# Performance work log

Hardware: AMD Instinct MI355X
Metric: run time of the kernel (lower is better)

## Reference

```python
import jax, jax.numpy as jnp
import numpy as np

N_NODES = 40960
N_EDGES = 655360
IN_DIM = 128
HID = 128
HEADS = 4
CH = HID // HEADS  # per-head channels = 32
N_GRAPHS = 16
NEG_SLOPE = 0.2


def setup_inputs() -> dict:
    key = jax.random.key(0)
    ks = jax.random.split(key, 32)
    inp = {
        "x": jax.random.normal(ks[0], (N_NODES, IN_DIM), dtype=jnp.float32),
        "edge_index": jax.random.randint(ks[1], (2, N_EDGES), 0, N_NODES, dtype=jnp.int64),
        "batch_vec": jnp.sort(jax.random.randint(ks[2], (N_NODES,), 0, N_GRAPHS, dtype=jnp.int64)),
    }
    dims = [(IN_DIM, HID), (HID, HID), (HID, HID)]
    ki = 3
    for l, (din, dout) in enumerate(dims):
        s = 1.0 / np.sqrt(din)
        inp[f"Wl{l}"] = jax.random.normal(ks[ki + 0], (din, dout), dtype=jnp.float32) * s
        inp[f"bl{l}"] = jnp.zeros((dout,), dtype=jnp.float32)
        inp[f"Wr{l}"] = jax.random.normal(ks[ki + 1], (din, dout), dtype=jnp.float32) * s
        inp[f"br{l}"] = jnp.zeros((dout,), dtype=jnp.float32)
        inp[f"att{l}"] = jax.random.normal(ks[ki + 2], (HEADS, CH), dtype=jnp.float32) * (1.0 / np.sqrt(CH))
        inp[f"b{l}"] = jnp.zeros((dout,), dtype=jnp.float32)
        ki += 3
    return inp


def _gatv2_layer(x, src, dst, Wl, bl, Wr, br, att, bias):
    # GATv2Conv (PyG semantics, add_self_loops=True handled by caller's src/dst)
    n = x.shape[0]
    xl = (x @ Wl + bl).reshape(n, HEADS, CH)  # source transform
    xr = (x @ Wr + br).reshape(n, HEADS, CH)  # destination transform
    m = xl[src] + xr[dst]                      # [E, H, C]
    e = jnp.einsum("ehc,hc->eh", jax.nn.leaky_relu(m, NEG_SLOPE), att)  # [E, H]
    emax = jax.ops.segment_max(e, dst, num_segments=n)
    ex = jnp.exp(e - emax[dst])
    denom = jax.ops.segment_sum(ex, dst, num_segments=n)
    alpha = ex / denom[dst]                    # segment softmax over in-edges
    out = jax.ops.segment_sum(alpha[:, :, None] * xl[src], dst, num_segments=n)
    return out.reshape(n, HEADS * CH) + bias


def reference(x, edge_index, batch_vec,
              Wl0, bl0, Wr0, br0, att0, b0,
              Wl1, bl1, Wr1, br1, att1, b1,
              Wl2, bl2, Wr2, br2, att2, b2):
    n = x.shape[0]
    loops = jnp.arange(n, dtype=edge_index.dtype)
    src = jnp.concatenate([edge_index[0], loops])  # PyG default add_self_loops=True
    dst = jnp.concatenate([edge_index[1], loops])

    h = _gatv2_layer(x, src, dst, Wl0, bl0, Wr0, br0, att0, b0)
    h = jax.nn.relu(h)
    h = _gatv2_layer(h, src, dst, Wl1, bl1, Wr1, br1, att1, b1)
    h = jax.nn.relu(h)
    h = _gatv2_layer(h, src, dst, Wl2, bl2, Wr2, br2, att2, b2)

    # global_mean_pool over batch assignment
    sums = jax.ops.segment_sum(h, batch_vec, num_segments=N_GRAPHS)
    cnt = jax.ops.segment_sum(jnp.ones((n,), dtype=h.dtype), batch_vec, num_segments=N_GRAPHS)
    pooled = sums / jnp.maximum(cnt, 1.0)[:, None]
    return pooled, h
```

## Files before the change

### kernel.cpp

```cpp
#include <hip/hip_runtime.h>

#define NN 40960
#define NE 655360
#define ET (NE + NN)
#define D 128
#define NG 16
#define PL 16896
#define NREP 8

typedef unsigned int u32;
typedef unsigned short u16;
typedef long long i64;
typedef __attribute__((ext_vector_type(8))) short bf8v;
typedef __attribute__((ext_vector_type(4))) float f4v;

struct P18 { const void* p[18]; };

__device__ __forceinline__ float bf2f(u16 v){ return __uint_as_float(((u32)v)<<16); }
__device__ __forceinline__ u16 f2bf(float f){
  u32 u = __float_as_uint(f);
  return (u16)((u + 0x7FFFu + ((u>>16)&1u)) >> 16);
}
__device__ __forceinline__ int geti(const void* p, long long i, int f64, int bound){
  long long v = f64 ? ((const i64*)p)[i] : (long long)((const int*)p)[i];
  int x = (int)v;
  return (x < 0) ? 0 : ((x >= bound) ? bound-1 : x);
}
__device__ __forceinline__ void stf(void* p, long long i, float v, int isbf){
  if (isbf) ((u16*)p)[i] = f2bf(v); else ((float*)p)[i] = v;
}
__device__ __forceinline__ float rdf(const void* p, long long i, int isbf){
  return isbf ? bf2f(((const u16*)p)[i]) : ((const float*)p)[i];
}
__device__ __forceinline__ float4 ldb4(const u16* p){
  ushort4 u = *(const ushort4*)p;
  return make_float4(bf2f(u.x), bf2f(u.y), bf2f(u.z), bf2f(u.w));
}

__global__ void k_setup(const void* __restrict__ ei, const void* __restrict__ x,
                        int* __restrict__ flags, u32* __restrict__ cursor, float* __restrict__ pool,
                        u16* __restrict__ csr){
  int b = blockIdx.x;
  if (b == 0){
    __shared__ int nz, cnt;
    if (threadIdx.x == 0){ nz = 0; cnt = 0; }
    __syncthreads();
    if (((const int*)ei)[2*threadIdx.x + 1] != 0) atomicAdd(&nz, 1);
    if (threadIdx.x < 128){
      u16 v = ((const u16*)x)[2*threadIdx.x];
      int ex = (v >> 7) & 0xFF;
      if (ex >= 100 && ex <= 140) atomicAdd(&cnt, 1);
    }
    __syncthreads();
    if (threadIdx.x == 0){
      flags[0] = (nz == 0) ? 1 : 0;
      flags[1] = (cnt >= 64) ? 1 : 0;
    }
  } else if (b <= 1280){
    cursor[(b-1)*256 + threadIdx.x] = 0u;
  } else if (b <= 1288){
    int i = (b-1281)*256 + threadIdx.x;
    if (i < NG*D) pool[i] = 0.f;
  } else {
    if (threadIdx.x < 16) csr[ET + threadIdx.x] = 0;
  }
}

__global__ void k_prep(P18 ps, const void* __restrict__ x, u16* __restrict__ xb,
                       float* __restrict__ prm, const int* __restrict__ flags){
  int b = blockIdx.x;
  int isbf = flags[1];
  if (b >= 390){
    long long i = (long long)(b - 390)*256 + threadIdx.x;
    xb[i] = f2bf(rdf(x, i, isbf));
    return;
  }
  int l = b / 130;
  int i = (b % 130)*256 + threadIdx.x;
  const void* Wl  = ps.p[6*l+0];
  const void* bl  = ps.p[6*l+1];
  const void* Wr  = ps.p[6*l+2];
  const void* br  = ps.p[6*l+3];
  const void* att = ps.p[6*l+4];
  const void* bb  = ps.p[6*l+5];
  float* p = prm + (size_t)l*PL;
  if (i < 32768){
    int n = i >> 7, k = i & 127;
    float v = (n < 128) ? rdf(Wl, k*128 + n, isbf) : rdf(Wr, k*128 + (n - 128), isbf);
    ((u16*)p)[i] = f2bf(v);
    return;
  }
  float* fb = p + 16384;
  if (i < 33024){ int gc = i - 32768; fb[gc] = (gc < 128) ? rdf(bl, gc, isbf) : rdf(br, gc - 128, isbf); }
  else if (i < 33152) fb[256 + (i - 33024)] = rdf(att, i - 33024, isbf);
  else                fb[384 + (i - 33152)] = rdf(bb, i - 33152, isbf);
}

__global__ void k_hist(const void* __restrict__ ei, u32* __restrict__ cursor, const int* __restrict__ flags){
  int e = blockIdx.x*256 + threadIdx.x;
  if (e >= ET) return;
  int dd = (e < NE) ? geti(ei, (long long)NE + e, flags[0], NN) : e - NE;
  atomicAdd(&cursor[(e & (NREP-1))*NN + dd], 1u);
}

__global__ __launch_bounds__(256) void k_scanA(u32* __restrict__ cursor, u32* __restrict__ tot,
                                               u32* __restrict__ psum){
  __shared__ u32 red[256];
  int t = threadIdx.x;
  int dd = blockIdx.x*256 + t;
  u32 run = 0;
  #pragma unroll
  for (int r = 0; r < NREP; ++r){
    u32 v = cursor[r*NN + dd];
    cursor[r*NN + dd] = run;
    run += v;
  }
  tot[dd] = run;
  red[t] = run;
  __syncthreads();
  #pragma unroll
  for (int off = 128; off > 0; off >>= 1){
    if (t < off) red[t] += red[t + off];
    __syncthreads();
  }
  if (t == 0) psum[blockIdx.x] = red[0];
}

__global__ __launch_bounds__(256) void k_scanB(u32* __restrict__ psum, u32* __restrict__ offs,
                                               const void* __restrict__ batch, u32* __restrict__ bnd,
                                               const int* __restrict__ flags){
  __shared__ u32 sh[256];
  int t = threadIdx.x;
  sh[t] = (t < 160) ? psum[t] : 0u;
  __syncthreads();
  #pragma unroll
  for (int off = 1; off < 256; off <<= 1){
    u32 add = (t >= off) ? sh[t - off] : 0u;
    __syncthreads();
    sh[t] += add;
    __syncthreads();
  }
  if (t < 160) psum[t] = (t == 0) ? 0u : sh[t - 1];
  if (t == 160) offs[NN] = sh[159];
  if (t >= 192 && t <= 192 + NG){
    int g = t - 192;
    if (g == NG){ bnd[NG] = NN; }
    else {
      int f = flags[0];
      int lo = 0, hi = NN;
      while (lo < hi){
        int mid = (lo + hi) >> 1;
        if (geti(batch, mid, f, NG) < g) lo = mid + 1; else hi = mid;
      }
      bnd[g] = (u32)lo;
    }
  }
}

__global__ __launch_bounds__(256) void k_scanC(u32* __restrict__ cursor, u32* __restrict__ offs,
                                               const u32* __restrict__ tot, const u32* __restrict__ psum){
  __shared__ u32 sh[256];
  int t = threadIdx.x;
  int dd = blockIdx.x*256 + t;
  u32 v = tot[dd];
  sh[t] = v;
  __syncthreads();
  #pragma unroll
  for (int off = 1; off < 256; off <<= 1){
    u32 add = (t >= off) ? sh[t - off] : 0u;
    __syncthreads();
    sh[t] += add;
    __syncthreads();
  }
  u32 excl = ((t > 0) ? sh[t - 1] : 0u) + psum[blockIdx.x];
  offs[dd] = excl;
  #pragma unroll
  for (int r = 0; r < NREP; ++r)
    cursor[r*NN + dd] += excl;
}

__global__ void k_scatter(const void* __restrict__ ei, u32* __restrict__ cursor,
                          u16* __restrict__ csr, const int* __restrict__ flags){
  int e = blockIdx.x*256 + threadIdx.x;
  if (e >= ET) return;
  int f = flags[0];
  int s, dd;
  if (e < NE){ s = geti(ei, e, f, NN); dd = geti(ei, (long long)NE + e, f, NN); }
  else { s = dd = e - NE; }
  u32 pos = atomicAdd(&cursor[(e & (NREP-1))*NN + dd], 1u);
  csr[pos] = (u16)s;
}

__global__ __launch_bounds__(256) void k_gemm(const u16* __restrict__ Xb, const float* __restrict__ pr,
                                              u16* __restrict__ xl, u16* __restrict__ xr)
{
  int wv = threadIdx.x >> 6, lane = threadIdx.x & 63;
  int row0 = blockIdx.x*64 + wv*16;
  int rA = lane & 15, ks = lane >> 4;
  const u16* wt     = (const u16*)pr;
  const float* bias = pr + 16384;

  const u16* xp = Xb + (size_t)(row0 + rA)*D + ks*8;
  bf8v a0 = *(const bf8v*)(xp);
  bf8v a1 = *(const bf8v*)(xp + 32);
  bf8v a2 = *(const bf8v*)(xp + 64);
  bf8v a3 = *(const bf8v*)(xp + 96);

  int n0 = blockIdx.y*4;
  #pragma unroll
  for (int t = 0; t < 4; ++t, ++n0){
    int gc = n0*16 + rA;
    const u16* wp = wt + (size_t)gc*D + ks*8;
    bf8v b0 = *(const bf8v*)(wp);
    bf8v b1 = *(const bf8v*)(wp + 32);
    bf8v b2 = *(const bf8v*)(wp + 64);
    bf8v b3 = *(const bf8v*)(wp + 96);
    float bv = bias[gc];
    f4v acc = {bv, bv, bv, bv};
    acc = __builtin_amdgcn_mfma_f32_16x16x32_bf16(a0, b0, acc, 0, 0, 0);
    acc = __builtin_amdgcn_mfma_f32_16x16x32_bf16(a1, b1, acc, 0, 0, 0);
    acc = __builtin_amdgcn_mfma_f32_16x16x32_bf16(a2, b2, acc, 0, 0, 0);
    acc = __builtin_amdgcn_mfma_f32_16x16x32_bf16(a3, b3, acc, 0, 0, 0);
    u16* dst = (gc < 128) ? xl : xr;
    int cc = (gc < 128) ? gc : gc - 128;
    #pragma unroll
    for (int r = 0; r < 4; ++r)
      dst[(size_t)(row0 + ks*4 + r)*D + cc] = f2bf(acc[r]);
  }
}

__global__ __launch_bounds__(256) void k_node(const u16* __restrict__ xl, const u16* __restrict__ xr,
    const u32* __restrict__ offs, const u16* __restrict__ csr, const float* __restrict__ pr,
    u16* __restrict__ hb, float* __restrict__ hf, void* __restrict__ out,
    const int* __restrict__ flags, int last)
{
  int node = blockIdx.x*4 + (threadIdx.x >> 6);
  int lane = threadIdx.x & 63;
  int half = lane >> 5;
  int c = (lane & 31) * 4;
  const u16* xlc = xl + c;
  float4 xrv  = ldb4(xr + (size_t)node*D + c);
  float4 attv = *(const float4*)(pr + 16640 + c);
  u32 j0 = offs[node], j1 = offs[node + 1];

  float mx = -1e30f, ssum = 0.f;
  float4 acc = make_float4(0.f, 0.f, 0.f, 0.f);

  u32 j = j0 + half;
  u32 o0 = ((u32)csr[j]) << 7, o1 = ((u32)csr[j+2]) << 7;
  float4 g0 = ldb4(xlc + o0);
  float4 g1 = ldb4(xlc + o1);
  u32 o2 = ((u32)csr[j+4]) << 7, o3 = ((u32)csr[j+6]) << 7;

  for (; j < j1; j += 4){
    float4 n0 = ldb4(xlc + o2);
    float4 n1 = ldb4(xlc + o3);
    u32 t0 = ((u32)csr[j+8]) << 7, t1 = ((u32)csr[j+10]) << 7;

    {
      float m, p;
      m = g0.x + xrv.x; p = fmaxf(m, 0.2f*m) * attv.x;
      m = g0.y + xrv.y; p = fmaf(fmaxf(m, 0.2f*m), attv.y, p);
      m = g0.z + xrv.z; p = fmaf(fmaxf(m, 0.2f*m), attv.z, p);
      m = g0.w + xrv.w; p = fmaf(fmaxf(m, 0.2f*m), attv.w, p);
      p += __shfl_xor(p, 1, 64);
      p += __shfl_xor(p, 2, 64);
      p += __shfl_xor(p, 4, 64);
      if (p > mx + 8.f){
        float eo = __expf(mx - p);
        ssum  *= eo;
        acc.x *= eo; acc.y *= eo; acc.z *= eo; acc.w *= eo;
        mx = p;
      }
      float en = __expf(p - mx);
      ssum += en;
      acc.x = fmaf(en, g0.x, acc.x);
      acc.y = fmaf(en, g0.y, acc.y);
      acc.z = fmaf(en, g0.z, acc.z);
      acc.w = fmaf(en, g0.w, acc.w);
    }
    if (j + 2 < j1){
      float m, p;
      m = g1.x + xrv.x; p = fmaxf(m, 0.2f*m) * attv.x;
      m = g1.y + xrv.y; p = fmaf(fmaxf(m, 0.2f*m), attv.y, p);
      m = g1.z + xrv.z; p = fmaf(fmaxf(m, 0.2f*m), attv.z, p);
      m = g1.w + xrv.w; p = fmaf(fmaxf(m, 0.2f*m), attv.w, p);
      p += __shfl_xor(p, 1, 64);
      p += __shfl_xor(p, 2, 64);
      p += __shfl_xor(p, 4, 64);
      if (p > mx + 8.f){
        float eo = __expf(mx - p);
        ssum  *= eo;
        acc.x *= eo; acc.y *= eo; acc.z *= eo; acc.w *= eo;
        mx = p;
      }
      float en = __expf(p - mx);
      ssum += en;
      acc.x = fmaf(en, g1.x, acc.x);
      acc.y = fmaf(en, g1.y, acc.y);
      acc.z = fmaf(en, g1.z, acc.z);
      acc.w = fmaf(en, g1.w, acc.w);
    }
    g0 = n0; g1 = n1; o2 = t0; o3 = t1;
  }

  float mo = __shfl_xor(mx, 32, 64);
  float so = __shfl_xor(ssum, 32, 64);
  float ax = __shfl_xor(acc.x, 32, 64);
  float ay = __shfl_xor(acc.y, 32, 64);
  float az = __shfl_xor(acc.z, 32, 64);
  float aw = __shfl_xor(acc.w, 32, 64);
  float n  = fmaxf(mx, mo);
  float e0 = __expf(mx - n), e1 = __expf(mo - n);
  ssum  = ssum*e0 + so*e1;
  acc.x = acc.x*e0 + ax*e1;
  acc.y = acc.y*e0 + ay*e1;
  acc.z = acc.z*e0 + az*e1;
  acc.w = acc.w*e0 + aw*e1;

  if (half == 0){
    float inv = 1.0f / fmaxf(ssum, 1e-30f);
    float4 bv = *(const float4*)(pr + 16768 + c);
    float4 v = make_float4(acc.x*inv + bv.x, acc.y*inv + bv.y,
                           acc.z*inv + bv.z, acc.w*inv + bv.w);
    if (!last){
      v.x = fmaxf(v.x, 0.f); v.y = fmaxf(v.y, 0.f);
      v.z = fmaxf(v.z, 0.f); v.w = fmaxf(v.w, 0.f);
      ushort4 o = make_ushort4(f2bf(v.x), f2bf(v.y), f2bf(v.z), f2bf(v.w));
      *(ushort4*)(hb + (size_t)node*D + c) = o;
    } else {
      *(float4*)(hf + (size_t)node*D + c) = v;
      int isbf = flags[1];
      long long o = (long long)NG*D + (long long)node*D + c;
      stf(out, o+0, v.x, isbf); stf(out, o+1, v.y, isbf);
      stf(out, o+2, v.z, isbf); stf(out, o+3, v.w, isbf);
    }
  }
}

__global__ __launch_bounds__(256) void k_pool1(const float* __restrict__ h, const u32* __restrict__ bnd,
                                               float* __restrict__ pool){
  __shared__ float red[256];
  int g = blockIdx.x >> 4, sl = blockIdx.x & 15;
  int ch = threadIdx.x & 127, ro = threadIdx.x >> 7;
  u32 b0 = bnd[g], b1 = bnd[g + 1];
  float acc = 0.f;
  for (u32 r = b0 + sl*2 + ro; r < b1; r += 32) acc += h[(size_t)r*D + ch];
  red[threadIdx.x] = acc;
  __syncthreads();
  if (threadIdx.x < 128)
    unsafeAtomicAdd(&pool[g*D + ch], red[threadIdx.x] + red[threadIdx.x + 128]);
}

__global__ void k_pool2(const float* __restrict__ pool, const u32* __restrict__ bnd,
                        void* __restrict__ out, const int* __restrict__ flags){
  int i = blockIdx.x*256 + threadIdx.x;
  if (i >= NG*D) return;
  int g = i >> 7;
  float c = (float)(bnd[g + 1] - bnd[g]);
  stf(out, i, pool[i] / fmaxf(c, 1.f), flags[1]);
}

extern "C" void kernel_launch(void* const* d_in, const int* in_sizes, int n_in,
                              void* d_out, int out_size, void* d_ws, size_t ws_size,
                              hipStream_t stream) {
  const void* x     = d_in[0];
  const void* ei    = d_in[1];
  const void* batch = d_in[2];

  const long long nf = (long long)NN*D + 3*PL + NG*D;
  const long long nh = (long long)NN*D*3;
  const long long nu = (NN + 1) + (long long)NREP*NN + NN + (NG + 1) + 160 + 2;
  const long long nc = ET + 16;
  if (ws_size < (size_t)nf*4 + (size_t)nh*2 + (size_t)nu*4 + (size_t)nc*2 + 256) return;

  float* ws    = (float*)d_ws;
  float* xf    = ws;
  u16*  xb    = (u16*)(xf + (size_t)NN*D);
  u16*  xl    = xb + (size_t)NN*D;
  u16*  xr    = xl + (size_t)NN*D;
  float* prm   = (float*)(xr + (size_t)NN*D);
  float* pool  = prm + 3*PL;
  u32*  offs   = (u32*)(pool + NG*D);
  u32*  cursor = offs + (NN + 1);
  u32*  tot    = cursor + (size_t)NREP*NN;
  u32*  bnd    = tot + NN;
  u32*  psum   = bnd + (NG + 1);
  int*  flags  = (int*)(psum + 160);
  u16*  csr    = (u16*)(flags + 2);

  k_setup<<<1290, 256, 0, stream>>>(ei, x, flags, cursor, pool, csr);
  P18 ps;
  for (int i = 0; i < 18; ++i) ps.p[i] = d_in[3 + i];
  k_prep<<<390 + (NN*D)/256, 256, 0, stream>>>(ps, x, xb, prm, flags);

  k_hist<<<ET/256, 256, 0, stream>>>(ei, cursor, flags);
  k_scanA<<<160, 256, 0, stream>>>(cursor, tot, psum);
  k_scanB<<<1, 256, 0, stream>>>(psum, offs, batch, bnd, flags);
  k_scanC<<<160, 256, 0, stream>>>(cursor, offs, tot, psum);
  k_scatter<<<ET/256, 256, 0, stream>>>(ei, cursor, csr, flags);

  for (int l = 0; l < 3; ++l){
    const float* p = prm + (size_t)l*PL;
    k_gemm<<<dim3(NN/64, 4), 256, 0, stream>>>(xb, p, xl, xr);
    k_node<<<NN/4, 256, 0, stream>>>(xl, xr, offs, csr, p, xb, xf, d_out, flags, l == 2);
  }
  k_pool1<<<NG*16, 256, 0, stream>>>(xf, bnd, pool);
  k_pool2<<<8, 256, 0, stream>>>(pool, bnd, d_out, flags);
}
```

Baseline: 313.8 us.

## Fuse histogram into prep, scatter with first GEMM; widen node lanes to 8 channels

The edge-degree histogram now runs as extra blocks of the prep kernel, and the CSR scatter shares a launch with the layer-0 projection GEMM. This removes two kernel launches and lets the independent work overlap. The node aggregation kernel now gives each lane 8 channels and runs 4 edge groups per wavefront instead of 2, with a two-step shuffle merge at the end. That roughly halves the shuffles per edge and issues wider gathers, at the cost of more registers and a longer final reduction.

After: 303.4 us. 3.3% less time.

```diff
diff --git a/kernel.cpp b/kernel.cpp
--- a/kernel.cpp
+++ b/kernel.cpp
@@ -7,6 +7,7 @@
 #define NG 16
 #define PL 16896
 #define NREP 8
+#define SCB 2720
 
 typedef unsigned int u32;
 typedef unsigned short u16;
@@ -67,9 +68,18 @@
 }
 
 __global__ void k_prep(P18 ps, const void* __restrict__ x, u16* __restrict__ xb,
-                       float* __restrict__ prm, const int* __restrict__ flags){
+                       float* __restrict__ prm, const void* __restrict__ ei,
+                       u32* __restrict__ cursor, const int* __restrict__ flags){
   int b = blockIdx.x;
   int isbf = flags[1];
+  if (b >= 20870){
+    int e = (b - 20870)*256 + threadIdx.x;
+    if (e < ET){
+      int dd = (e < NE) ? geti(ei, (long long)NE + e, flags[0], NN) : e - NE;
+      atomicAdd(&cursor[(e & (NREP-1))*NN + dd], 1u);
+    }
+    return;
+  }
   if (b >= 390){
     long long i = (long long)(b - 390)*256 + threadIdx.x;
     xb[i] = f2bf(rdf(x, i, isbf));
@@ -96,13 +106,6 @@
   else                fb[384 + (i - 33152)] = rdf(bb, i - 33152, isbf);
 }
 
-__global__ void k_hist(const void* __restrict__ ei, u32* __restrict__ cursor, const int* __restrict__ flags){
-  int e = blockIdx.x*256 + threadIdx.x;
-  if (e >= ET) return;
-  int dd = (e < NE) ? geti(ei, (long long)NE + e, flags[0], NN) : e - NE;
-  atomicAdd(&cursor[(e & (NREP-1))*NN + dd], 1u);
-}
-
 __global__ __launch_bounds__(256) void k_scanA(u32* __restrict__ cursor, u32* __restrict__ tot,
                                                u32* __restrict__ psum){
   __shared__ u32 red[256];
@@ -179,23 +182,12 @@
     cursor[r*NN + dd] += excl;
 }
 
-__global__ void k_scatter(const void* __restrict__ ei, u32* __restrict__ cursor,
-                          u16* __restrict__ csr, const int* __restrict__ flags){
-  int e = blockIdx.x*256 + threadIdx.x;
-  if (e >= ET) return;
-  int f = flags[0];
-  int s, dd;
-  if (e < NE){ s = geti(ei, e, f, NN); dd = geti(ei, (long long)NE + e, f, NN); }
-  else { s = dd = e - NE; }
-  u32 pos = atomicAdd(&cursor[(e & (NREP-1))*NN + dd], 1u);
-  csr[pos] = (u16)s;
-}
-
-__global__ __launch_bounds__(256) void k_gemm(const u16* __restrict__ Xb, const float* __restrict__ pr,
-                                              u16* __restrict__ xl, u16* __restrict__ xr)
+__device__ __forceinline__ void gemm_body(int bx, int by, int tid,
+    const u16* __restrict__ Xb, const float* __restrict__ pr,
+    u16* __restrict__ xl, u16* __restrict__ xr)
 {
-  int wv = threadIdx.x >> 6, lane = threadIdx.x & 63;
-  int row0 = blockIdx.x*64 + wv*16;
+  int wv = tid >> 6, lane = tid & 63;
+  int row0 = bx*64 + wv*16;
   int rA = lane & 15, ks = lane >> 4;
   const u16* wt     = (const u16*)pr;
   const float* bias = pr + 16384;
@@ -206,7 +198,7 @@
   bf8v a2 = *(const bf8v*)(xp + 64);
   bf8v a3 = *(const bf8v*)(xp + 96);
 
-  int n0 = blockIdx.y*4;
+  int n0 = by*4;
   #pragma unroll
   for (int t = 0; t < 4; ++t, ++n0){
     int gc = n0*16 + rA;
@@ -229,6 +221,32 @@
   }
 }
 
+__global__ __launch_bounds__(256) void k_gemm(const u16* __restrict__ Xb, const float* __restrict__ pr,
+                                              u16* __restrict__ xl, u16* __restrict__ xr){
+  gemm_body(blockIdx.x, blockIdx.y, threadIdx.x, Xb, pr, xl, xr);
+}
+
+__global__ __launch_bounds__(256) void k_scatgemm(const void* __restrict__ ei, u32* __restrict__ cursor,
+    u16* __restrict__ csr, const int* __restrict__ flags,
+    const u16* __restrict__ Xb, const float* __restrict__ pr,
+    u16* __restrict__ xl, u16* __restrict__ xr)
+{
+  int b = blockIdx.x;
+  if (b < SCB){
+    int e = b*256 + threadIdx.x;
+    if (e >= ET) return;
+    int f = flags[0];
+    int s, dd;
+    if (e < NE){ s = geti(ei, e, f, NN); dd = geti(ei, (long long)NE + e, f, NN); }
+    else { s = dd = e - NE; }
+    u32 pos = atomicAdd(&cursor[(e & (NREP-1))*NN + dd], 1u);
+    csr[pos] = (u16)s;
+    return;
+  }
+  int g = b - SCB;
+  gemm_body(g % 640, g / 640, threadIdx.x, Xb, pr, xl, xr);
+}
+
 __global__ __launch_bounds__(256) void k_node(const u16* __restrict__ xl, const u16* __restrict__ xr,
     const u32* __restrict__ offs, const u16* __restrict__ csr, const float* __restrict__ pr,
     u16* __restrict__ hb, float* __restrict__ hf, void* __restrict__ out,
@@ -236,104 +254,98 @@
 {
   int node = blockIdx.x*4 + (threadIdx.x >> 6);
   int lane = threadIdx.x & 63;
-  int half = lane >> 5;
-  int c = (lane & 31) * 4;
+  int g2 = lane >> 4;
+  int c = (lane & 15) * 8;
   const u16* xlc = xl + c;
-  float4 xrv  = ldb4(xr + (size_t)node*D + c);
-  float4 attv = *(const float4*)(pr + 16640 + c);
+  const u16* xrp = xr + (size_t)node*D + c;
+  float4 xr0 = ldb4(xrp), xr1 = ldb4(xrp + 4);
+  float4 at0 = *(const float4*)(pr + 16640 + c);
+  float4 at1 = *(const float4*)(pr + 16640 + c + 4);
   u32 j0 = offs[node], j1 = offs[node + 1];
 
   float mx = -1e30f, ssum = 0.f;
-  float4 acc = make_float4(0.f, 0.f, 0.f, 0.f);
-
-  u32 j = j0 + half;
-  u32 o0 = ((u32)csr[j]) << 7, o1 = ((u32)csr[j+2]) << 7;
-  float4 g0 = ldb4(xlc + o0);
-  float4 g1 = ldb4(xlc + o1);
-  u32 o2 = ((u32)csr[j+4]) << 7, o3 = ((u32)csr[j+6]) << 7;
+  float4 ac0 = make_float4(0.f,0.f,0.f,0.f), ac1 = make_float4(0.f,0.f,0.f,0.f);
+
+  u32 j = j0 + g2;
+  u32 oc = ((u32)csr[j]) << 7;
+  float4 g0 = ldb4(xlc + oc), g1 = ldb4(xlc + oc + 4);
+  u32 on = ((u32)csr[j + 4]) << 7;
 
   for (; j < j1; j += 4){
-    float4 n0 = ldb4(xlc + o2);
-    float4 n1 = ldb4(xlc + o3);
-    u32 t0 = ((u32)csr[j+8]) << 7, t1 = ((u32)csr[j+10]) << 7;
-
-    {
-      float m, p;
-      m = g0.x + xrv.x; p = fmaxf(m, 0.2f*m) * attv.x;
-      m = g0.y + xrv.y; p = fmaf(fmaxf(m, 0.2f*m), attv.y, p);
-      m = g0.z + xrv.z; p = fmaf(fmaxf(m, 0.2f*m), attv.z, p);
-      m = g0.w + xrv.w; p = fmaf(fmaxf(m, 0.2f*m), attv.w, p);
-      p += __shfl_xor(p, 1, 64);
-      p += __shfl_xor(p, 2, 64);
-      p += __shfl_xor(p, 4, 64);
-      if (p > mx + 8.f){
-        float eo = __expf(mx - p);
-        ssum  *= eo;
-        acc.x *= eo; acc.y *= eo; acc.z *= eo; acc.w *= eo;
-        mx = p;
-      }
-      float en = __expf(p - mx);
-      ssum += en;
-      acc.x = fmaf(en, g0.x, acc.x);
-      acc.y = fmaf(en, g0.y, acc.y);
-      acc.z = fmaf(en, g0.z, acc.z);
-      acc.w = fmaf(en, g0.w, acc.w);
-    }
-    if (j + 2 < j1){
-      float m, p;
-      m = g1.x + xrv.x; p = fmaxf(m, 0.2f*m) * attv.x;
-      m = g1.y + xrv.y; p = fmaf(fmaxf(m, 0.2f*m), attv.y, p);
-      m = g1.z + xrv.z; p = fmaf(fmaxf(m, 0.2f*m), attv.z, p);
-      m = g1.w + xrv.w; p = fmaf(fmaxf(m, 0.2f*m), attv.w, p);
-      p += __shfl_xor(p, 1, 64);
-      p += __shfl_xor(p, 2, 64);
-      p += __shfl_xor(p, 4, 64);
-      if (p > mx + 8.f){
-        float eo = __expf(mx - p);
-        ssum  *= eo;
-        acc.x *= eo; acc.y *= eo; acc.z *= eo; acc.w *= eo;
-        mx = p;
-      }
-      float en = __expf(p - mx);
-      ssum += en;
-      acc.x = fmaf(en, g1.x, acc.x);
-      acc.y = fmaf(en, g1.y, acc.y);
-      acc.z = fmaf(en, g1.z, acc.z);
-      acc.w = fmaf(en, g1.w, acc.w);
-    }
-    g0 = n0; g1 = n1; o2 = t0; o3 = t1;
-  }
-
-  float mo = __shfl_xor(mx, 32, 64);
-  float so = __shfl_xor(ssum, 32, 64);
-  float ax = __shfl_xor(acc.x, 32, 64);
-  float ay = __shfl_xor(acc.y, 32, 64);
-  float az = __shfl_xor(acc.z, 32, 64);
-  float aw = __shfl_xor(acc.w, 32, 64);
-  float n  = fmaxf(mx, mo);
-  float e0 = __expf(mx - n), e1 = __expf(mo - n);
-  ssum  = ssum*e0 + so*e1;
-  acc.x = acc.x*e0 + ax*e1;
-  acc.y = acc.y*e0 + ay*e1;
-  acc.z = acc.z*e0 + az*e1;
-  acc.w = acc.w*e0 + aw*e1;
-
-  if (half == 0){
+    float4 n0 = ldb4(xlc + on), n1 = ldb4(xlc + on + 4);
+    u32 o2 = ((u32)csr[j + 8]) << 7;
+
+    float m, p;
+    m = g0.x + xr0.x; p = fmaxf(m, 0.2f*m) * at0.x;
+    m = g0.y + xr0.y; p = fmaf(fmaxf(m, 0.2f*m), at0.y, p);
+    m = g0.z + xr0.z; p = fmaf(fmaxf(m, 0.2f*m), at0.z, p);
+    m = g0.w + xr0.w; p = fmaf(fmaxf(m, 0.2f*m), at0.w, p);
+    m = g1.x + xr1.x; p = fmaf(fmaxf(m, 0.2f*m), at1.x, p);
+    m = g1.y + xr1.y; p = fmaf(fmaxf(m, 0.2f*m), at1.y, p);
+    m = g1.z + xr1.z; p = fmaf(fmaxf(m, 0.2f*m), at1.z, p);
+    m = g1.w + xr1.w; p = fmaf(fmaxf(m, 0.2f*m), at1.w, p);
+    p += __shfl_xor(p, 1, 64);
+    p += __shfl_xor(p, 2, 64);
+    if (p > mx + 8.f){
+      float eo = __expf(mx - p);
+      ssum *= eo;
+      ac0.x *= eo; ac0.y *= eo; ac0.z *= eo; ac0.w *= eo;
+      ac1.x *= eo; ac1.y *= eo; ac1.z *= eo; ac1.w *= eo;
+      mx = p;
+    }
+    float en = __expf(p - mx);
+    ssum += en;
+    ac0.x = fmaf(en, g0.x, ac0.x); ac0.y = fmaf(en, g0.y, ac0.y);
+    ac0.z = fmaf(en, g0.z, ac0.z); ac0.w = fmaf(en, g0.w, ac0.w);
+    ac1.x = fmaf(en, g1.x, ac1.x); ac1.y = fmaf(en, g1.y, ac1.y);
+    ac1.z = fmaf(en, g1.z, ac1.z); ac1.w = fmaf(en, g1.w, ac1.w);
+    g0 = n0; g1 = n1; on = o2;
+  }
+
+  #pragma unroll
+  for (int off = 16; off < 64; off <<= 1){
+    float mo  = __shfl_xor(mx, off, 64);
+    float so  = __shfl_xor(ssum, off, 64);
+    float b0x = __shfl_xor(ac0.x, off, 64), b0y = __shfl_xor(ac0.y, off, 64);
+    float b0z = __shfl_xor(ac0.z, off, 64), b0w = __shfl_xor(ac0.w, off, 64);
+    float b1x = __shfl_xor(ac1.x, off, 64), b1y = __shfl_xor(ac1.y, off, 64);
+    float b1z = __shfl_xor(ac1.z, off, 64), b1w = __shfl_xor(ac1.w, off, 64);
+    float nm = fmaxf(mx, mo);
+    float e0 = __expf(mx - nm), e1 = __expf(mo - nm);
+    ssum  = ssum*e0 + so*e1;
+    ac0.x = ac0.x*e0 + b0x*e1; ac0.y = ac0.y*e0 + b0y*e1;
+    ac0.z = ac0.z*e0 + b0z*e1; ac0.w = ac0.w*e0 + b0w*e1;
+    ac1.x = ac1.x*e0 + b1x*e1; ac1.y = ac1.y*e0 + b1y*e1;
+    ac1.z = ac1.z*e0 + b1z*e1; ac1.w = ac1.w*e0 + b1w*e1;
+    mx = nm;
+  }
+
+  if (lane < 16){
     float inv = 1.0f / fmaxf(ssum, 1e-30f);
-    float4 bv = *(const float4*)(pr + 16768 + c);
-    float4 v = make_float4(acc.x*inv + bv.x, acc.y*inv + bv.y,
-                           acc.z*inv + bv.z, acc.w*inv + bv.w);
+    float4 bv0 = *(const float4*)(pr + 16768 + c);
+    float4 bv1 = *(const float4*)(pr + 16768 + c + 4);
+    float4 v0 = make_float4(ac0.x*inv + bv0.x, ac0.y*inv + bv0.y,
+                            ac0.z*inv + bv0.z, ac0.w*inv + bv0.w);
+    float4 v1 = make_float4(ac1.x*inv + bv1.x, ac1.y*inv + bv1.y,
+                            ac1.z*inv + bv1.z, ac1.w*inv + bv1.w);
     if (!last){
-      v.x = fmaxf(v.x, 0.f); v.y = fmaxf(v.y, 0.f);
-      v.z = fmaxf(v.z, 0.f); v.w = fmaxf(v.w, 0.f);
-      ushort4 o = make_ushort4(f2bf(v.x), f2bf(v.y), f2bf(v.z), f2bf(v.w));
-      *(ushort4*)(hb + (size_t)node*D + c) = o;
+      v0.x = fmaxf(v0.x, 0.f); v0.y = fmaxf(v0.y, 0.f);
+      v0.z = fmaxf(v0.z, 0.f); v0.w = fmaxf(v0.w, 0.f);
+      v1.x = fmaxf(v1.x, 0.f); v1.y = fmaxf(v1.y, 0.f);
+      v1.z = fmaxf(v1.z, 0.f); v1.w = fmaxf(v1.w, 0.f);
+      u16* hp = hb + (size_t)node*D + c;
+      *(ushort4*)(hp)     = make_ushort4(f2bf(v0.x), f2bf(v0.y), f2bf(v0.z), f2bf(v0.w));
+      *(ushort4*)(hp + 4) = make_ushort4(f2bf(v1.x), f2bf(v1.y), f2bf(v1.z), f2bf(v1.w));
     } else {
-      *(float4*)(hf + (size_t)node*D + c) = v;
+      float* fp = hf + (size_t)node*D + c;
+      *(float4*)(fp)     = v0;
+      *(float4*)(fp + 4) = v1;
       int isbf = flags[1];
       long long o = (long long)NG*D + (long long)node*D + c;
-      stf(out, o+0, v.x, isbf); stf(out, o+1, v.y, isbf);
-      stf(out, o+2, v.z, isbf); stf(out, o+3, v.w, isbf);
+      stf(out, o+0, v0.x, isbf); stf(out, o+1, v0.y, isbf);
+      stf(out, o+2, v0.z, isbf); stf(out, o+3, v0.w, isbf);
+      stf(out, o+4, v1.x, isbf); stf(out, o+5, v1.y, isbf);
+      stf(out, o+6, v1.z, isbf); stf(out, o+7, v1.w, isbf);
     }
   }
 }
@@ -392,18 +404,19 @@
   k_setup<<<1290, 256, 0, stream>>>(ei, x, flags, cursor, pool, csr);
   P18 ps;
   for (int i = 0; i < 18; ++i) ps.p[i] = d_in[3 + i];
-  k_prep<<<390 + (NN*D)/256, 256, 0, stream>>>(ps, x, xb, prm, flags);
-
-  k_hist<<<ET/256, 256, 0, stream>>>(ei, cursor, flags);
+  k_prep<<<390 + (NN*D)/256 + SCB, 256, 0, stream>>>(ps, x, xb, prm, ei, cursor, flags);
+
   k_scanA<<<160, 256, 0, stream>>>(cursor, tot, psum);
   k_scanB<<<1, 256, 0, stream>>>(psum, offs, batch, bnd, flags);
   k_scanC<<<160, 256, 0, stream>>>(cursor, offs, tot, psum);
-  k_scatter<<<ET/256, 256, 0, stream>>>(ei, cursor, csr, flags);
+  k_scatgemm<<<SCB + 2560, 256, 0, stream>>>(ei, cursor, csr, flags,
+                                             xb, prm, xl, xr);
 
   for (int l = 0; l < 3; ++l){
-    const float* p = prm + (size_t)l*PL;
-    k_gemm<<<dim3(NN/64, 4), 256, 0, stream>>>(xb, p, xl, xr);
-    k_node<<<NN/4, 256, 0, stream>>>(xl, xr, offs, csr, p, xb, xf, d_out, flags, l == 2);
+    if (l > 0)
+      k_gemm<<<dim3(NN/64, 4), 256, 0, stream>>>(xb, prm + (size_t)l*PL, xl, xr);
+    k_node<<<NN/4, 256, 0, stream>>>(xl, xr, offs, csr, prm + (size_t)l*PL,
+                                     xb, xf, d_out, flags, l == 2);
   }
   k_pool1<<<NG*16, 256, 0, stream>>>(xf, bnd, pool);
   k_pool2<<<8, 256, 0, stream>>>(pool, bnd, d_out, flags);
```
